# Kernel optimization log

Measured on AMD Instinct MI355X. Metric: run time of the kernel, lower is better.

The kernel has to match this reference:

```python
import jax, jax.numpy as jnp
import numpy as np

NUM_EMBEDDINGS = 1024
EMBEDDING_DIM = 64
BETA = 0.25


def setup_inputs() -> dict:
    key = jax.random.key(0)
    k1, k2 = jax.random.split(key)
    inputs = jax.random.normal(k1, (16, 64, 64, 64), dtype=jnp.float32)
    # tf.random_uniform_initializer default: uniform in [-0.05, 0.05]
    embedding = jax.random.uniform(k2, (NUM_EMBEDDINGS, EMBEDDING_DIM),
                                   dtype=jnp.float32, minval=-0.05, maxval=0.05)
    return {"inputs": inputs, "embedding": embedding}


def reference(inputs, embedding):
    input_shape = inputs.shape
    flat = inputs.reshape(-1, EMBEDDING_DIM)  # [N, D]
    # squared L2 distances to each codebook entry: [N, K]
    distances = (jnp.sum(flat * flat, axis=1, keepdims=True)
                 + jnp.sum(embedding * embedding, axis=1)
                 - 2.0 * jnp.einsum('nd,kd->nk', flat, embedding))
    idx = jnp.argmin(distances, axis=1)  # [N]
    # one-hot @ embedding is just a gather of codebook rows
    quantized = embedding[idx].reshape(input_shape)

    # Keras MSE reduces over the last axis (per-element losses), then
    # add_loss aggregates; we take the mean to get the scalar VQ loss.
    commitment_loss = jnp.mean(jnp.mean(
        (jax.lax.stop_gradient(quantized) - inputs) ** 2, axis=-1))
    codebook_loss = jnp.mean(jnp.mean(
        (quantized - jax.lax.stop_gradient(inputs)) ** 2, axis=-1))
    loss = codebook_loss + BETA * commitment_loss

    # straight-through estimator
    quantized_ste = inputs + jax.lax.stop_gradient(quantized - inputs)
    return quantized_ste, loss
```

## Files before the change

### kernel.cpp

```cpp
#include <hip/hip_runtime.h>
#include <math.h>

#define NROWS 65536
#define D     64
#define K     1024
#define NCT   8
#define BR    128
#define BC    128
#define BETA  0.25f
#define SCALE 1024.0f
#define THR   200.0f
#define FXS   1048576.0

typedef _Float16 half8  __attribute__((ext_vector_type(8)));
typedef float    f32x4  __attribute__((ext_vector_type(4)));
typedef unsigned long long u64;

#define WS_BP   0u
#define WS_EN   (256u*1024)
#define WS_EN2  (260u*1024)
#define WS_LIST (264u*1024)
#define WS_CNT  (WS_LIST + 256u*1024)
#define WS_ERR  (WS_CNT + 128u)

static __device__ __forceinline__ unsigned ordf(float f) {
    unsigned b = __float_as_uint(f);
    return (b & 0x80000000u) ? ~b : (b | 0x80000000u);
}
static __device__ __forceinline__ void gload_lds16(const void* g, void* l) {
    __builtin_amdgcn_global_load_lds(
        (const __attribute__((address_space(1))) unsigned*)g,
        (__attribute__((address_space(3))) unsigned*)l,
        16, 0, 0);
}

__global__ __launch_bounds__(256) void vq_prep(const float* __restrict__ emb,
                                               float* __restrict__ enorm,
                                               float* __restrict__ enorm2,
                                               char* __restrict__ Bp,
                                               unsigned* __restrict__ counter,
                                               u64* __restrict__ errAcc) {
    if (blockIdx.x == 0 && threadIdx.x == 0) { counter[0] = 0u; errAcc[0] = 0ull; }
    int k = blockIdx.x * 256 + threadIdx.x;
    if (k >= K) return;
    const int ct = k >> 7, r = k & 127;
    char* base = Bp + (size_t)ct * 32768 + (size_t)r * 128;
    const float4* e4 = (const float4*)(emb + (size_t)k * D);
    float s = 0.f;
    #pragma unroll
    for (int c = 0; c < 8; ++c) {
        float4 ea = e4[2 * c], eb = e4[2 * c + 1];
        s += ea.x * ea.x + ea.y * ea.y + ea.z * ea.z + ea.w * ea.w;
        s += eb.x * eb.x + eb.y * eb.y + eb.z * eb.z + eb.w * eb.w;
        float sc[8] = {ea.x * SCALE, ea.y * SCALE, ea.z * SCALE, ea.w * SCALE,
                       eb.x * SCALE, eb.y * SCALE, eb.z * SCALE, eb.w * SCALE};
        half8 hh, hl;
        #pragma unroll
        for (int e = 0; e < 8; ++e) {
            _Float16 h = (_Float16)sc[e];
            hh[e] = h;
            hl[e] = (_Float16)(sc[e] - (float)h);
        }
        int off = ((c ^ (r & 7)) << 4);
        *(half8*)(base + off)         = hh;
        *(half8*)(base + 16384 + off) = hl;
    }
    enorm[k]  = s;
    enorm2[k] = s * (SCALE * SCALE);
}

__global__ __launch_bounds__(256, 2) void vq_gemm(const float* __restrict__ x,
                                                  const char* __restrict__ Bp,
                                                  const float* __restrict__ emb,
                                                  const float* __restrict__ enorm2,
                                                  float* __restrict__ out,
                                                  unsigned* __restrict__ list,
                                                  unsigned* __restrict__ counter,
                                                  u64* __restrict__ errAcc) {
    __shared__ __align__(16) char bufB[2][32768];
    __shared__ float redE[256];

    const int tid  = threadIdx.x;
    const int lane = tid & 63, w = tid >> 6;
    const int fr   = lane & 15;
    const int kg   = lane >> 4;
    const int rb   = (int)blockIdx.x * BR;

    const float4* x4 = (const float4*)x;
    half8 ah[2][2], al[2][2];
    #pragma unroll
    for (int fi = 0; fi < 2; ++fi) {
        #pragma unroll
        for (int kk = 0; kk < 2; ++kk) {
            int row = rb + w * 32 + fi * 16 + fr;
            float4 v0 = x4[(size_t)row * 16 + kk * 8 + kg * 2];
            float4 v1 = x4[(size_t)row * 16 + kk * 8 + kg * 2 + 1];
            float sc[8] = {v0.x * SCALE, v0.y * SCALE, v0.z * SCALE, v0.w * SCALE,
                           v1.x * SCALE, v1.y * SCALE, v1.z * SCALE, v1.w * SCALE};
            #pragma unroll
            for (int e = 0; e < 8; ++e) {
                _Float16 h = (_Float16)sc[e];
                ah[fi][kk][e] = h;
                al[fi][kk][e] = (_Float16)(sc[e] - (float)h);
            }
        }
    }

    {
        const char* gsrc = Bp + (size_t)w * 8192 + (size_t)lane * 16;
        char* ldst = &bufB[0][w * 8192];
        #pragma unroll
        for (int j = 0; j < 8; ++j)
            gload_lds16(gsrc + j * 1024, ldst + j * 1024);
    }

    float d1[2][4], d2[2][4];
    int   i1[2][4];
    #pragma unroll
    for (int fi = 0; fi < 2; ++fi)
        #pragma unroll
        for (int rg = 0; rg < 4; ++rg) {
            d1[fi][rg] = 3.4e38f; d2[fi][rg] = 3.4e38f; i1[fi][rg] = 0;
        }

    for (int ct = 0; ct < NCT; ++ct) {
        const int  cb  = ct * BC;
        const int  buf = ct & 1;
        __syncthreads();

        if (ct < NCT - 1) {
            const char* gsrc = Bp + (size_t)(ct + 1) * 32768 + (size_t)w * 8192
                             + (size_t)lane * 16;
            char* ldst = &bufB[buf ^ 1][w * 8192];
            #pragma unroll
            for (int j = 0; j < 8; ++j)
                gload_lds16(gsrc + j * 1024, ldst + j * 1024);
        }

        float en2f[8];
        #pragma unroll
        for (int ci = 0; ci < 8; ++ci)
            en2f[ci] = enorm2[cb + ci * 16 + fr];
        const int idxb = cb + fr;

        const char* bb = &bufB[buf][0];

        #pragma unroll
        for (int g = 0; g < 2; ++g) {
            f32x4 acc[2][4];
            #pragma unroll
            for (int fi = 0; fi < 2; ++fi)
                #pragma unroll
                for (int i = 0; i < 4; ++i) acc[fi][i] = (f32x4){0.f, 0.f, 0.f, 0.f};

            #pragma unroll
            for (int kk = 0; kk < 2; ++kk) {
                const int chunk = ((kk * 4 + kg) ^ (fr & 7)) << 4;
                half8 bf[4];
                #pragma unroll
                for (int i = 0; i < 4; ++i)
                    bf[i] = *(const half8*)(bb + ((g * 4 + i) * 16 + fr) * 128 + chunk);
                #pragma unroll
                for (int fi = 0; fi < 2; ++fi)
                    #pragma unroll
                    for (int i = 0; i < 4; ++i)
                        acc[fi][i] = __builtin_amdgcn_mfma_f32_16x16x32_f16(ah[fi][kk], bf[i], acc[fi][i], 0, 0, 0);
                #pragma unroll
                for (int fi = 0; fi < 2; ++fi)
                    #pragma unroll
                    for (int i = 0; i < 4; ++i)
                        acc[fi][i] = __builtin_amdgcn_mfma_f32_16x16x32_f16(al[fi][kk], bf[i], acc[fi][i], 0, 0, 0);
                #pragma unroll
                for (int i = 0; i < 4; ++i)
                    bf[i] = *(const half8*)(bb + 16384 + ((g * 4 + i) * 16 + fr) * 128 + chunk);
                #pragma unroll
                for (int fi = 0; fi < 2; ++fi)
                    #pragma unroll
                    for (int i = 0; i < 4; ++i)
                        acc[fi][i] = __builtin_amdgcn_mfma_f32_16x16x32_f16(ah[fi][kk], bf[i], acc[fi][i], 0, 0, 0);
            }

            #pragma unroll
            for (int fi = 0; fi < 2; ++fi) {
                #pragma unroll
                for (int rg = 0; rg < 4; ++rg) {
                    #pragma unroll
                    for (int i = 0; i < 4; ++i) {
                        float d  = fmaf(-2.f, acc[fi][i][rg], en2f[g * 4 + i]);
                        int  idx = idxb + (g * 4 + i) * 16;
                        bool lt  = d < d1[fi][rg];
                        d2[fi][rg] = fminf(fmaxf(d1[fi][rg], d), d2[fi][rg]);
                        i1[fi][rg] = lt ? idx : i1[fi][rg];
                        d1[fi][rg] = fminf(d1[fi][rg], d);
                    }
                }
            }
        }
    }

    const float4* e4g = (const float4*)emb;
    float4* o4 = (float4*)out;
    float errp = 0.f;
    #pragma unroll
    for (int fi = 0; fi < 2; ++fi) {
        #pragma unroll
        for (int rg = 0; rg < 4; ++rg) {
            float v1 = d1[fi][rg], v2 = d2[fi][rg];
            int   ii = i1[fi][rg];
            #pragma unroll
            for (int off = 8; off >= 1; off >>= 1) {
                float o1 = __shfl_xor(v1, off, 16);
                float o2 = __shfl_xor(v2, off, 16);
                int   oi = __shfl_xor(ii, off, 16);
                float loser = fmaxf(v1, o1);
                v2 = fminf(fminf(v2, o2), loser);
                bool bt = o1 < v1;
                v1 = fminf(v1, o1);
                ii = bt ? oi : ii;
            }
            int row = rb + w * 32 + fi * 16 + kg * 4 + rg;
            if (v2 - v1 > THR) {
                float4 q = e4g[(size_t)ii * 16 + fr];
                float4 v = x4[(size_t)row * 16 + fr];
                o4[(size_t)row * 16 + fr] = q;
                float ax = q.x - v.x, ay = q.y - v.y, az = q.z - v.z, aw = q.w - v.w;
                errp += ax * ax + ay * ay + az * az + aw * aw;
            } else if (fr == 0) {
                unsigned pos = atomicAdd(counter, 1u);
                list[pos] = (unsigned)row;
            }
        }
    }

    __syncthreads();
    redE[tid] = errp;
    __syncthreads();
    for (int s = 128; s > 0; s >>= 1) {
        if (tid < s) redE[tid] += redE[tid + s];
        __syncthreads();
    }
    if (tid == 0)
        atomicAdd(errAcc, (u64)((double)redE[0] * FXS + 0.5));
}

__global__ __launch_bounds__(256) void vq_fallback(const float* __restrict__ x,
                                                   const float* __restrict__ emb,
                                                   const float* __restrict__ enorm,
                                                   const unsigned* __restrict__ list,
                                                   const unsigned* __restrict__ counter,
                                                   float* __restrict__ out,
                                                   u64* __restrict__ errAcc) {
    __shared__ float4 xr[16];
    __shared__ u64 red[256];
    __shared__ float errv[16];
    const int tid = threadIdx.x;
    const unsigned total = counter[0];
    u64 qerr = 0ull;
    for (unsigned i = blockIdx.x; i < total; i += gridDim.x) {
        const int n = (int)list[i];
        __syncthreads();
        if (tid < 16) xr[tid] = ((const float4*)x)[(size_t)n * 16 + tid];
        __syncthreads();
        float xnorm = 0.f;
        #pragma unroll
        for (int q = 0; q < 16; ++q) {
            float4 v = xr[q];
            xnorm += v.x * v.x + v.y * v.y + v.z * v.z + v.w * v.w;
        }
        u64 best = ~0ull;
        #pragma unroll
        for (int j = 0; j < 4; ++j) {
            int k = tid + j * 256;
            const float4* e4 = (const float4*)(emb + (size_t)k * D);
            float d0 = 0.f, d1v = 0.f, d2v = 0.f, d3v = 0.f;
            #pragma unroll
            for (int q = 0; q < 4; ++q) {
                float4 ea = e4[q*4+0], eb = e4[q*4+1], ec = e4[q*4+2], ed = e4[q*4+3];
                float4 va = xr[q*4+0], vb = xr[q*4+1], vc = xr[q*4+2], vd = xr[q*4+3];
                d0  = fmaf(va.w, ea.w, fmaf(va.z, ea.z, fmaf(va.y, ea.y, fmaf(va.x, ea.x, d0))));
                d1v = fmaf(vb.w, eb.w, fmaf(vb.z, eb.z, fmaf(vb.y, eb.y, fmaf(vb.x, eb.x, d1v))));
                d2v = fmaf(vc.w, ec.w, fmaf(vc.z, ec.z, fmaf(vc.y, ec.y, fmaf(vc.x, ec.x, d2v))));
                d3v = fmaf(vd.w, ed.w, fmaf(vd.z, ed.z, fmaf(vd.y, ed.y, fmaf(vd.x, ed.x, d3v))));
            }
            float dot  = (d0 + d1v) + (d2v + d3v);
            float dist = fmaf(-2.f, dot, xnorm + enorm[k]);
            u64 pk = ((u64)ordf(dist) << 32) | (unsigned)k;
            if (pk < best) best = pk;
        }
        red[tid] = best;
        __syncthreads();
        for (int s = 128; s > 0; s >>= 1) {
            if (tid < s) red[tid] = red[tid] < red[tid+s] ? red[tid] : red[tid+s];
            __syncthreads();
        }
        const int bi = (int)(red[0] & 0xFFFFFFFFu);
        if (tid < 16) {
            float4 q = ((const float4*)emb)[(size_t)bi * 16 + tid];
            float4 v = xr[tid];
            ((float4*)out)[(size_t)n * 16 + tid] = q;
            float ax = q.x - v.x, ay = q.y - v.y, az = q.z - v.z, aw = q.w - v.w;
            errv[tid] = ax * ax + ay * ay + az * az + aw * aw;
        }
        __syncthreads();
        if (tid == 0) {
            float re = 0.f;
            #pragma unroll
            for (int j = 0; j < 16; ++j) re += errv[j];
            qerr += (u64)((double)re * FXS + 0.5);
        }
    }
    if (tid == 0 && qerr) atomicAdd(errAcc, qerr);
}

__global__ __launch_bounds__(64) void vq_finish(const u64* __restrict__ errAcc,
                                                float* __restrict__ loss_out) {
    if (threadIdx.x == 0) {
        double s = (double)errAcc[0] / FXS;
        loss_out[0] = (float)((1.0 + (double)BETA) * s / (double)((size_t)NROWS * D));
    }
}

extern "C" void kernel_launch(void* const* d_in, const int* in_sizes, int n_in,
                              void* d_out, int out_size, void* d_ws, size_t ws_size,
                              hipStream_t stream) {
    const float* x   = (const float*)d_in[0];
    const float* emb = (const float*)d_in[1];
    float* out = (float*)d_out;
    char* ws = (char*)d_ws;

    char* Bp          = ws + WS_BP;
    float* enorm      = (float*)(ws + WS_EN);
    float* enorm2     = (float*)(ws + WS_EN2);
    unsigned* list    = (unsigned*)(ws + WS_LIST);
    unsigned* counter = (unsigned*)(ws + WS_CNT);
    u64* errAcc       = (u64*)(ws + WS_ERR);

    vq_prep<<<K / 256, 256, 0, stream>>>(emb, enorm, enorm2, Bp, counter, errAcc);
    vq_gemm<<<NROWS / BR, 256, 0, stream>>>(x, Bp, emb, enorm2, out, list, counter, errAcc);
    vq_fallback<<<128, 256, 0, stream>>>(x, emb, enorm, list, counter, out, errAcc);
    vq_finish<<<1, 64, 0, stream>>>(errAcc, out + (size_t)NROWS * D);
}
```

Baseline: 61.59 us.

## Read codebook fragments directly from global memory instead of LDS double buffering

The prep kernel now stores the split-fp16 codebook in a fragment-major layout, so each lane's MFMA B operand is one contiguous 16-byte global load. The GEMM kernel drops the shared-memory double buffer, the async global-to-LDS copies and the per-tile barriers, and loads B fragments straight from global memory, relying on the L2/L1 caches because every block rereads the small codebook. Freeing 64KB of LDS and removing the occupancy hint may let more waves run per CU. The cost is exposed global-load latency inside the MFMA loop with no explicit prefetch.

```diff
diff --git a/kernel.cpp b/kernel.cpp
--- a/kernel.cpp
+++ b/kernel.cpp
@@ -27,12 +27,6 @@
     unsigned b = __float_as_uint(f);
     return (b & 0x80000000u) ? ~b : (b | 0x80000000u);
 }
-static __device__ __forceinline__ void gload_lds16(const void* g, void* l) {
-    __builtin_amdgcn_global_load_lds(
-        (const __attribute__((address_space(1))) unsigned*)g,
-        (__attribute__((address_space(3))) unsigned*)l,
-        16, 0, 0);
-}
 
 __global__ __launch_bounds__(256) void vq_prep(const float* __restrict__ emb,
                                                float* __restrict__ enorm,
@@ -43,8 +37,10 @@
     if (blockIdx.x == 0 && threadIdx.x == 0) { counter[0] = 0u; errAcc[0] = 0ull; }
     int k = blockIdx.x * 256 + threadIdx.x;
     if (k >= K) return;
-    const int ct = k >> 7, r = k & 127;
-    char* base = Bp + (size_t)ct * 32768 + (size_t)r * 128;
+    const int ct  = k >> 7;
+    const int ci  = (k & 127) >> 4;
+    const int frk = k & 15;
+    char* tbase = Bp + (size_t)ct * 32768;
     const float4* e4 = (const float4*)(emb + (size_t)k * D);
     float s = 0.f;
     #pragma unroll
@@ -61,23 +57,23 @@
             hh[e] = h;
             hl[e] = (_Float16)(sc[e] - (float)h);
         }
-        int off = ((c ^ (r & 7)) << 4);
-        *(half8*)(base + off)         = hh;
-        *(half8*)(base + 16384 + off) = hl;
+        const int kk = c >> 2, kg = c & 3;
+        char* dst = tbase + kk * 8192 + ci * 1024 + (kg * 16 + frk) * 16;
+        *(half8*)dst            = hh;
+        *(half8*)(dst + 16384)  = hl;
     }
     enorm[k]  = s;
     enorm2[k] = s * (SCALE * SCALE);
 }
 
-__global__ __launch_bounds__(256, 2) void vq_gemm(const float* __restrict__ x,
-                                                  const char* __restrict__ Bp,
-                                                  const float* __restrict__ emb,
-                                                  const float* __restrict__ enorm2,
-                                                  float* __restrict__ out,
-                                                  unsigned* __restrict__ list,
-                                                  unsigned* __restrict__ counter,
-                                                  u64* __restrict__ errAcc) {
-    __shared__ __align__(16) char bufB[2][32768];
+__global__ __launch_bounds__(256) void vq_gemm(const float* __restrict__ x,
+                                               const char* __restrict__ Bp,
+                                               const float* __restrict__ emb,
+                                               const float* __restrict__ enorm2,
+                                               float* __restrict__ out,
+                                               unsigned* __restrict__ list,
+                                               unsigned* __restrict__ counter,
+                                               u64* __restrict__ errAcc) {
     __shared__ float redE[256];
 
     const int tid  = threadIdx.x;
@@ -106,14 +102,6 @@
         }
     }
 
-    {
-        const char* gsrc = Bp + (size_t)w * 8192 + (size_t)lane * 16;
-        char* ldst = &bufB[0][w * 8192];
-        #pragma unroll
-        for (int j = 0; j < 8; ++j)
-            gload_lds16(gsrc + j * 1024, ldst + j * 1024);
-    }
-
     float d1[2][4], d2[2][4];
     int   i1[2][4];
     #pragma unroll
@@ -124,18 +112,8 @@
         }
 
     for (int ct = 0; ct < NCT; ++ct) {
-        const int  cb  = ct * BC;
-        const int  buf = ct & 1;
-        __syncthreads();
-
-        if (ct < NCT - 1) {
-            const char* gsrc = Bp + (size_t)(ct + 1) * 32768 + (size_t)w * 8192
-                             + (size_t)lane * 16;
-            char* ldst = &bufB[buf ^ 1][w * 8192];
-            #pragma unroll
-            for (int j = 0; j < 8; ++j)
-                gload_lds16(gsrc + j * 1024, ldst + j * 1024);
-        }
+        const int cb = ct * BC;
+        const char* tb = Bp + (size_t)ct * 32768 + (size_t)lane * 16;
 
         float en2f[8];
         #pragma unroll
@@ -143,8 +121,6 @@
             en2f[ci] = enorm2[cb + ci * 16 + fr];
         const int idxb = cb + fr;
 
-        const char* bb = &bufB[buf][0];
-
         #pragma unroll
         for (int g = 0; g < 2; ++g) {
             f32x4 acc[2][4];
@@ -155,11 +131,11 @@
 
             #pragma unroll
             for (int kk = 0; kk < 2; ++kk) {
-                const int chunk = ((kk * 4 + kg) ^ (fr & 7)) << 4;
+                const char* kb = tb + kk * 8192;
                 half8 bf[4];
                 #pragma unroll
                 for (int i = 0; i < 4; ++i)
-                    bf[i] = *(const half8*)(bb + ((g * 4 + i) * 16 + fr) * 128 + chunk);
+                    bf[i] = *(const half8*)(kb + (g * 4 + i) * 1024);
                 #pragma unroll
                 for (int fi = 0; fi < 2; ++fi)
                     #pragma unroll
@@ -172,7 +148,7 @@
                         acc[fi][i] = __builtin_amdgcn_mfma_f32_16x16x32_f16(al[fi][kk], bf[i], acc[fi][i], 0, 0, 0);
                 #pragma unroll
                 for (int i = 0; i < 4; ++i)
-                    bf[i] = *(const half8*)(bb + 16384 + ((g * 4 + i) * 16 + fr) * 128 + chunk);
+                    bf[i] = *(const half8*)(kb + 16384 + (g * 4 + i) * 1024);
                 #pragma unroll
                 for (int fi = 0; fi < 2; ++fi)
                     #pragma unroll
```

After: 77.06 us, median of 2. 1.25x slower.
